# Kernel optimization log

Hardware: AMD Instinct MI355X
Metric: run time of the kernel (lower is better)

## Reference

```python
import jax, jax.numpy as jnp
import numpy as np

T, B, E, H = 2048, 2, 1024, 16
D = E // H

def setup_inputs() -> dict:
    key = jax.random.key(0)
    ks = jax.random.split(key, 5)
    s = 1.0 / np.sqrt(E)  # keep projection weights at sane scale
    return {
        "query": jax.random.normal(ks[0], (T, B, E), jnp.float32),
        "Wq": jax.random.normal(ks[1], (E, E), jnp.float32) * s,
        "bq": jnp.zeros((E,), jnp.float32),
        "Wk": jax.random.normal(ks[2], (E, E), jnp.float32) * s,
        "bk": jnp.zeros((E,), jnp.float32),
        "Wv": jax.random.normal(ks[3], (E, E), jnp.float32) * s,
        "bv": jnp.zeros((E,), jnp.float32),
        "Wo": jax.random.normal(ks[4], (E, E), jnp.float32) * s,
        "bo": jnp.zeros((E,), jnp.float32),
    }

def reference(query, Wq, bq, Wk, bk, Wv, bv, Wo, bo):
    # query: [T, B, E] (fairseq time-first). self-attention path.
    scaling = D ** -0.5
    q = (query @ Wq.T + bq) * scaling          # [T,B,E]
    k = query @ Wk.T + bk                      # [T,B,E]
    v = query @ Wv.T + bv                      # [T,B,E]
    # split heads: [T,B,H,D]
    q = q.reshape(T, B, H, D)
    k = k.reshape(T, B, H, D)
    v = v.reshape(T, B, H, D)
    # attention scores [B,H,T,S]
    scores = jnp.einsum("tbhd,sbhd->bhts", q, k)
    probs = jax.nn.softmax(scores, axis=-1)
    # weighted values -> [T,B,H,D]
    attn = jnp.einsum("bhts,sbhd->tbhd", probs, v).reshape(T, B, E)
    return attn @ Wo.T + bo                    # [T,B,E]
```

## Files before the change

kernel.cpp:

```cpp
#include <hip/hip_runtime.h>
#include <hip/hip_bf16.h>

#define T_DIM 2048

typedef __attribute__((ext_vector_type(8))) short short8_t;
typedef short8_t __attribute__((may_alias)) short8_a;
typedef __attribute__((ext_vector_type(4))) short short4_t;
typedef short4_t __attribute__((may_alias)) short4_a;
typedef __attribute__((ext_vector_type(4))) float f32x4;
typedef __attribute__((ext_vector_type(16))) float f32x16;
typedef __attribute__((ext_vector_type(4))) float float4_t;
typedef float4_t __attribute__((may_alias)) float4_a;
typedef __attribute__((ext_vector_type(4))) unsigned int u32x4;

__device__ __forceinline__ short f2bf(float f) {
    unsigned int u = __builtin_bit_cast(unsigned int, f);
    unsigned int r = (u + 0x7fffu + ((u >> 16) & 1u)) >> 16;
    return (short)r;
}

__device__ __forceinline__ void gl_lds16(const short* g, short* l) {
    __builtin_amdgcn_global_load_lds(
        (const __attribute__((address_space(1))) void*)g,
        (__attribute__((address_space(3))) void*)l, 16, 0, 0);
}

__global__ __launch_bounds__(256) void cvt_all(const float* __restrict__ query,
                                               const float* __restrict__ Wq,
                                               const float* __restrict__ Wk,
                                               const float* __restrict__ Wv,
                                               const float* __restrict__ Wo,
                                               short* __restrict__ out) {
    const int bx = blockIdx.x;
    const int i = bx * 2048 + threadIdx.x * 8;
    const float* s;
    if (bx < 2048) {
        s = query + i;
    } else {
        int j = i - 4194304;
        int wsel = j >> 20;
        const float* wp = wsel == 0 ? Wq : (wsel == 1 ? Wk : (wsel == 2 ? Wv : Wo));
        s = wp + (j & 1048575);
    }
    float4_a a = *(const float4_a*)s;
    float4_a b = *(const float4_a*)(s + 4);
    short8_a r;
    r[0] = f2bf(a[0]); r[1] = f2bf(a[1]); r[2] = f2bf(a[2]); r[3] = f2bf(a[3]);
    r[4] = f2bf(b[0]); r[5] = f2bf(b[1]); r[6] = f2bf(b[2]); r[7] = f2bf(b[3]);
    *(short8_a*)(out + i) = r;
}

template <int BM, int BN, int MODE>
__global__ __launch_bounds__(256) void gemm_lds(const short* __restrict__ A,
                                                const short* __restrict__ W,
                                                const float* __restrict__ b0,
                                                const float* __restrict__ b1,
                                                const float* __restrict__ b2,
                                                short* __restrict__ o0,
                                                short* __restrict__ o1,
                                                short* __restrict__ o2,
                                                float* __restrict__ of) {
    constexpr int FM = BM / 32;
    constexpr int FN = BN / 32;
    __shared__ short As[BM * 32];
    __shared__ short Bs[BN * 32];

    const int tid = threadIdx.x;
    const int l = tid & 63, w = tid >> 6;
    const int wm = w >> 1, wn = w & 1;

    const int nbx = gridDim.x;
    const int nb = nbx * gridDim.y;
    const int bid = blockIdx.x + nbx * blockIdx.y;
    const int swz = (bid & 7) * (nb >> 3) + (bid >> 3);
    const int bx = swz % nbx, by = swz / nbx;

    const int m0 = by * BM, n0 = bx * BN;
    const int l15 = l & 15, l4 = l >> 4;
    const int lr = l >> 2, lc = (l & 3) * 8;

    f32x4 acc[FM][FN];
#pragma unroll
    for (int i = 0; i < FM; i++)
#pragma unroll
        for (int j = 0; j < FN; j++) {
            f32x4 z = {0.f, 0.f, 0.f, 0.f};
            acc[i][j] = z;
        }

    const short* Ab = A + (m0 + lr) * 1024 + lc;
    const short* Wb = W + (n0 + lr) * 1024 + lc;

    for (int k0 = 0; k0 < 1024; k0 += 32) {
#pragma unroll
        for (int j = 0; j < BM / 64; j++) {
            int base = (j * 4 + w) * 16;
            gl_lds16(Ab + base * 1024 + k0, &As[base * 32]);
        }
#pragma unroll
        for (int j = 0; j < BN / 64; j++) {
            int base = (j * 4 + w) * 16;
            gl_lds16(Wb + base * 1024 + k0, &Bs[base * 32]);
        }
        __syncthreads();

        short8_t af[FM], bf[FN];
#pragma unroll
        for (int m = 0; m < FM; m++)
            af[m] = *(const short8_a*)&As[(wm * (BM / 2) + m * 16 + l15) * 32 + l4 * 8];
#pragma unroll
        for (int n = 0; n < FN; n++)
            bf[n] = *(const short8_a*)&Bs[(wn * (BN / 2) + n * 16 + l15) * 32 + l4 * 8];
#pragma unroll
        for (int m = 0; m < FM; m++)
#pragma unroll
            for (int n = 0; n < FN; n++)
                acc[m][n] = __builtin_amdgcn_mfma_f32_16x16x32_bf16(af[m], bf[n], acc[m][n], 0, 0, 0);
        __syncthreads();
    }

    if (MODE == 3) {
#pragma unroll
        for (int n = 0; n < FN; n++) {
            int col = n0 + wn * (BN / 2) + n * 16 + l15;
            float bv = b0[col];
#pragma unroll
            for (int m = 0; m < FM; m++)
#pragma unroll
                for (int i = 0; i < 4; i++) {
                    int row = m0 + wm * (BM / 2) + m * 16 + l4 * 4 + i;
                    of[row * 1024 + col] = acc[m][n][i] + bv;
                }
        }
    } else {
        const int proj = n0 >> 10;
        const float* bias = proj == 0 ? b0 : (proj == 1 ? b1 : b2);
        short* outp = proj == 0 ? o0 : (proj == 1 ? o1 : o2);
#pragma unroll
        for (int n = 0; n < FN; n++) {
            int cw = (n0 + wn * (BN / 2) + n * 16 + l15) & 1023;
            float bv = bias[cw];
            int h = cw >> 6, d = cw & 63;
#pragma unroll
            for (int m = 0; m < FM; m++)
#pragma unroll
                for (int i = 0; i < 4; i++) {
                    int row = m0 + wm * (BM / 2) + m * 16 + l4 * 4 + i;
                    float v = acc[m][n][i] + bv;
                    if (proj == 0) v *= 0.18033688011112042f;
                    int bb = row & 1, t = row >> 1;
                    if (proj == 2)
                        outp[((bb * 16 + h) * 64 + d) * 2048 + t] = f2bf(v);
                    else
                        outp[((bb * 16 + h) * 2048 + t) * 64 + d] = f2bf(v);
                }
        }
    }
}

__global__ __launch_bounds__(512, 4) void flash_attn(const short* __restrict__ Q,
                                                     const short* __restrict__ K,
                                                     const short* __restrict__ Vt,
                                                     short* __restrict__ O) {
    __shared__ short Ks[4][64 * 64];
    __shared__ short Vs[4][64 * 64];

    const int tid = threadIdx.x, l = tid & 63, w = tid >> 6;
    const int w4 = w >> 1, g = w & 1;
    const int l31 = l & 31, hi = l >> 5;
    const int e = l31 & 7;

    const int bid = blockIdx.x + (blockIdx.y << 4);
    const int swz = (bid & 7) * 64 + (bid >> 3);
    const int qt = swz & 15, bh = swz >> 4;

    const int b = bh >> 4, hh = bh & 15;
    const int qrow = qt * 128 + w4 * 32 + l31;

    const short* Qp = Q + bh * (T_DIM * 64);
    const short* Kp = K + bh * (T_DIM * 64);
    const short* Vp = Vt + bh * (64 * T_DIM);

    short8_t qf[4];
#pragma unroll
    for (int c = 0; c < 4; c++)
        qf[c] = *(const short8_a*)&Qp[qrow * 64 + c * 16 + hi * 8];

    f32x16 oacc[2];
    f32x16 lacc;
#pragma unroll
    for (int i = 0; i < 16; i++) { oacc[0][i] = 0.f; oacc[1][i] = 0.f; lacc[i] = 0.f; }

    short8_t ones;
#pragma unroll
    for (int j = 0; j < 8; j++) ones[j] = (short)0x3F80;

    const int lrow = l >> 3;
    const int lch = (l & 7) ^ (lrow & 7);
    const int wq = w & 3;
    const int j0 = 2 * wq, j1 = 2 * wq + 1;
    const short* sg0;
    const short* sg1;
    if (w < 4) {
        sg0 = Kp + (j0 * 8 + lrow) * 64 + lch * 8;
        sg1 = Kp + (j1 * 8 + lrow) * 64 + lch * 8;
    } else {
        sg0 = Vp + (j0 * 8 + lrow) * 2048 + lch * 8;
        sg1 = Vp + (j1 * 8 + lrow) * 2048 + lch * 8;
    }

    auto stage = [&](int t) {
        const int buf = t & 3;
        if (w < 4) {
            const int koff = t * 4096;
            gl_lds16(sg0 + koff, &Ks[buf][j0 * 512]);
            gl_lds16(sg1 + koff, &Ks[buf][j1 * 512]);
        } else {
            const int voff = t * 64;
            gl_lds16(sg0 + voff, &Vs[buf][j0 * 512]);
            gl_lds16(sg1 + voff, &Vs[buf][j1 * 512]);
        }
    };

    auto qk = [&](f32x16* st, int t) {
        const short* kc = &Ks[t & 3][0];
        f32x16 z;
#pragma unroll
        for (int i = 0; i < 16; i++) z[i] = 0.f;
        st[0] = z; st[1] = z;
#pragma unroll
        for (int c = 0; c < 4; c++) {
            short8_t kf0 = *(const short8_a*)&kc[(l31) * 64 + ((2 * c + hi) ^ e) * 8];
            short8_t kf1 = *(const short8_a*)&kc[(32 + l31) * 64 + ((2 * c + hi) ^ e) * 8];
            st[0] = __builtin_amdgcn_mfma_f32_32x32x16_bf16(kf0, qf[c], st[0], 0, 0, 0);
            st[1] = __builtin_amdgcn_mfma_f32_32x32x16_bf16(kf1, qf[c], st[1], 0, 0, 0);
        }
    };

    auto pv = [&](const short8_t* pf, int t) {
        const short* vc = &Vs[t & 3][0];
#pragma unroll
        for (int r = 0; r < 2; r++)
#pragma unroll
            for (int cc = 0; cc < 2; cc++) {
                short8_t p = pf[r * 2 + cc];
                lacc = __builtin_amdgcn_mfma_f32_32x32x16_bf16(ones, p, lacc, 0, 0, 0);
#pragma unroll
                for (int dd = 0; dd < 2; dd++) {
                    short8_t vf = *(const short8_a*)&vc[(dd * 32 + l31) * 64 +
                                                        ((4 * r + 2 * cc + hi) ^ e) * 8];
                    oacc[dd] = __builtin_amdgcn_mfma_f32_32x32x16_bf16(vf, p, oacc[dd], 0, 0, 0);
                }
            }
    };

    auto expack = [&](f32x16* st, short8_t* pf) {
#pragma unroll
        for (int r = 0; r < 2; r++) {
#pragma unroll
            for (int i = 0; i < 16; i++) st[r][i] = exp2f(st[r][i]);
            unsigned pk8[8];
#pragma unroll
            for (int u = 0; u < 8; u++) {
                unsigned t;
                asm("v_cvt_pk_bf16_f32 %0, %1, %2" : "=v"(t) : "v"(st[r][2 * u]), "v"(st[r][2 * u + 1]));
                pk8[u] = t;
            }
#pragma unroll
            for (int cc = 0; cc < 2; cc++) {
                unsigned A0 = pk8[4 * cc + 0], B0 = pk8[4 * cc + 2];
                unsigned A1 = pk8[4 * cc + 1], B1 = pk8[4 * cc + 3];
                asm("v_permlane32_swap_b32 %0, %1" : "+v"(A0), "+v"(B0));
                asm("v_permlane32_swap_b32 %0, %1" : "+v"(A1), "+v"(B1));
                u32x4 pu = {A0, A1, B0, B1};
                pf[r * 2 + cc] = __builtin_bit_cast(short8_t, pu);
            }
        }
    };

    stage(0);
    stage(1);

    f32x16 st[2];
    short8_t pf[4];

    for (int p = 0; p < 16; ++p) {
        __syncthreads();
        if (p < 15) { stage(2 * p + 2); stage(2 * p + 3); }
        const int t = 2 * p + g;
        __builtin_amdgcn_s_setprio(1);
        qk(st, t);
        __builtin_amdgcn_s_setprio(0);
        expack(st, pf);
        __builtin_amdgcn_s_setprio(1);
        pv(pf, t);
        __builtin_amdgcn_s_setprio(0);
    }

    __syncthreads();
    float* xo = (float*)&Ks[0][0];
    float* xml = (float*)&Vs[0][0];
    if (g == 1) {
#pragma unroll
        for (int dd = 0; dd < 2; dd++)
#pragma unroll
            for (int g4 = 0; g4 < 4; g4++) {
                f32x4 v = {oacc[dd][4 * g4], oacc[dd][4 * g4 + 1],
                           oacc[dd][4 * g4 + 2], oacc[dd][4 * g4 + 3]};
                *(float4_a*)&xo[w4 * 2048 + (dd * 4 + g4) * 256 + l * 4] = v;
            }
        xml[w4 * 64 + l] = lacc[0];
    }
    __syncthreads();
    if (g == 0) {
        float rl = 1.0f / (lacc[0] + xml[w4 * 64 + l]);
#pragma unroll
        for (int dd = 0; dd < 2; dd++)
#pragma unroll
            for (int g4 = 0; g4 < 4; g4++) {
                f32x4 o1 = *(const float4_a*)&xo[w4 * 2048 + (dd * 4 + g4) * 256 + l * 4];
                short4_t o4;
#pragma unroll
                for (int i = 0; i < 4; i++)
                    o4[i] = f2bf((oacc[dd][4 * g4 + i] + o1[i]) * rl);
                *(short4_a*)&O[(qrow * 2 + b) * 1024 + hh * 64 + dd * 32 + g4 * 8 + hi * 4] = o4;
            }
    }
}

extern "C" void kernel_launch(void* const* d_in, const int* in_sizes, int n_in,
                              void* d_out, int out_size, void* d_ws, size_t ws_size,
                              hipStream_t stream) {
    const float* query = (const float*)d_in[0];
    const float* Wq = (const float*)d_in[1];
    const float* bq = (const float*)d_in[2];
    const float* Wk = (const float*)d_in[3];
    const float* bk = (const float*)d_in[4];
    const float* Wv = (const float*)d_in[5];
    const float* bv = (const float*)d_in[6];
    const float* Wo = (const float*)d_in[7];
    const float* bo = (const float*)d_in[8];

    short* Xbf = (short*)d_ws;
    short* Wqb = Xbf + 4194304;
    short* Wkb = Wqb + 1048576;
    short* Wvb = Wkb + 1048576;
    short* Wob = Wvb + 1048576;
    short* Qb = Wob + 1048576;
    short* Kb = Qb + 4194304;
    short* Vtb = Kb + 4194304;
    short* attnb = Xbf;

    cvt_all<<<4096, 256, 0, stream>>>(query, Wq, Wk, Wv, Wo, Xbf);

    gemm_lds<128, 128, 4><<<dim3(24, 32), 256, 0, stream>>>(Xbf, Wqb, bq, bk, bv,
                                                            Qb, Kb, Vtb, nullptr);

    flash_attn<<<dim3(16, 32), 512, 0, stream>>>(Qb, Kb, Vtb, attnb);

    gemm_lds<64, 128, 3><<<dim3(8, 64), 256, 0, stream>>>(attnb, Wob, bo, nullptr, nullptr,
                                                          nullptr, nullptr, nullptr, (float*)d_out);
}
```

Measured before the change: 123.6 us.

## Pre-tile K/V into LDS-ready blocked layout and split QK into halves

The projection epilogue now writes K and V in a 64-row-tile, 8-element-chunked layout that matches the LDS fragment order. This lets flash attention stage tiles with contiguous global-to-LDS copies and read fragments without an XOR swizzle. The QK^T and exp/pack step is split into two 32-row halves that reuse one accumulator, which lowers register pressure. The risks are strided scattered global writes in the projection epilogue, possible LDS bank conflicts now that the swizzle is gone, and less MFMA overlap between the two halves.

```diff
diff --git a/kernel.cpp b/kernel.cpp
--- a/kernel.cpp
+++ b/kernel.cpp
@@ -149,10 +149,13 @@
                     float v = acc[m][n][i] + bv;
                     if (proj == 0) v *= 0.18033688011112042f;
                     int bb = row & 1, t = row >> 1;
-                    if (proj == 2)
-                        outp[((bb * 16 + h) * 64 + d) * 2048 + t] = f2bf(v);
+                    int bh = bb * 16 + h;
+                    if (proj == 0)
+                        outp[(bh * 2048 + t) * 64 + d] = f2bf(v);
+                    else if (proj == 1)
+                        outp[bh * 131072 + (t >> 6) * 4096 + (d >> 3) * 512 + (t & 63) * 8 + (d & 7)] = f2bf(v);
                     else
-                        outp[((bb * 16 + h) * 2048 + t) * 64 + d] = f2bf(v);
+                        outp[bh * 131072 + (t >> 6) * 4096 + ((t & 63) >> 3) * 512 + d * 8 + (t & 7)] = f2bf(v);
                 }
         }
     }
@@ -168,7 +171,6 @@
     const int tid = threadIdx.x, l = tid & 63, w = tid >> 6;
     const int w4 = w >> 1, g = w & 1;
     const int l31 = l & 31, hi = l >> 5;
-    const int e = l31 & 7;
 
     const int bid = blockIdx.x + (blockIdx.y << 4);
     const int swz = (bid & 7) * 64 + (bid >> 3);
@@ -178,8 +180,8 @@
     const int qrow = qt * 128 + w4 * 32 + l31;
 
     const short* Qp = Q + bh * (T_DIM * 64);
-    const short* Kp = K + bh * (T_DIM * 64);
-    const short* Vp = Vt + bh * (64 * T_DIM);
+    const short* Kp = K + bh * 131072;
+    const short* Vp = Vt + bh * 131072;
 
     short8_t qf[4];
 #pragma unroll
@@ -195,45 +197,58 @@
 #pragma unroll
     for (int j = 0; j < 8; j++) ones[j] = (short)0x3F80;
 
-    const int lrow = l >> 3;
-    const int lch = (l & 7) ^ (lrow & 7);
     const int wq = w & 3;
-    const int j0 = 2 * wq, j1 = 2 * wq + 1;
-    const short* sg0;
-    const short* sg1;
-    if (w < 4) {
-        sg0 = Kp + (j0 * 8 + lrow) * 64 + lch * 8;
-        sg1 = Kp + (j1 * 8 + lrow) * 64 + lch * 8;
-    } else {
-        sg0 = Vp + (j0 * 8 + lrow) * 2048 + lch * 8;
-        sg1 = Vp + (j1 * 8 + lrow) * 2048 + lch * 8;
-    }
+    const int p0 = 2 * wq, p1 = 2 * wq + 1;
+    const short* sgK0 = Kp + p0 * 512 + l * 8;
+    const short* sgK1 = Kp + p1 * 512 + l * 8;
+    const short* sgV0 = Vp + p0 * 512 + l * 8;
+    const short* sgV1 = Vp + p1 * 512 + l * 8;
 
     auto stage = [&](int t) {
-        const int buf = t & 3;
+        const int buf = t & 3, off = t * 4096;
         if (w < 4) {
-            const int koff = t * 4096;
-            gl_lds16(sg0 + koff, &Ks[buf][j0 * 512]);
-            gl_lds16(sg1 + koff, &Ks[buf][j1 * 512]);
+            gl_lds16(sgK0 + off, &Ks[buf][p0 * 512]);
+            gl_lds16(sgK1 + off, &Ks[buf][p1 * 512]);
         } else {
-            const int voff = t * 64;
-            gl_lds16(sg0 + voff, &Vs[buf][j0 * 512]);
-            gl_lds16(sg1 + voff, &Vs[buf][j1 * 512]);
+            gl_lds16(sgV0 + off, &Vs[buf][p0 * 512]);
+            gl_lds16(sgV1 + off, &Vs[buf][p1 * 512]);
         }
     };
 
-    auto qk = [&](f32x16* st, int t) {
+    auto qkhalf = [&](f32x16& s, int t, int r) {
         const short* kc = &Ks[t & 3][0];
-        f32x16 z;
-#pragma unroll
-        for (int i = 0; i < 16; i++) z[i] = 0.f;
-        st[0] = z; st[1] = z;
 #pragma unroll
         for (int c = 0; c < 4; c++) {
-            short8_t kf0 = *(const short8_a*)&kc[(l31) * 64 + ((2 * c + hi) ^ e) * 8];
-            short8_t kf1 = *(const short8_a*)&kc[(32 + l31) * 64 + ((2 * c + hi) ^ e) * 8];
-            st[0] = __builtin_amdgcn_mfma_f32_32x32x16_bf16(kf0, qf[c], st[0], 0, 0, 0);
-            st[1] = __builtin_amdgcn_mfma_f32_32x32x16_bf16(kf1, qf[c], st[1], 0, 0, 0);
+            short8_t kf = *(const short8_a*)&kc[(2 * c + hi) * 512 + (r * 32 + l31) * 8];
+            if (c == 0) {
+                f32x16 z;
+#pragma unroll
+                for (int i = 0; i < 16; i++) z[i] = 0.f;
+                s = __builtin_amdgcn_mfma_f32_32x32x16_bf16(kf, qf[0], z, 0, 0, 0);
+            } else {
+                s = __builtin_amdgcn_mfma_f32_32x32x16_bf16(kf, qf[c], s, 0, 0, 0);
+            }
+        }
+    };
+
+    auto expackhalf = [&](f32x16& s, short8_t* pf2) {
+#pragma unroll
+        for (int i = 0; i < 16; i++) s[i] = exp2f(s[i]);
+        unsigned pk8[8];
+#pragma unroll
+        for (int u = 0; u < 8; u++) {
+            unsigned t;
+            asm("v_cvt_pk_bf16_f32 %0, %1, %2" : "=v"(t) : "v"(s[2 * u]), "v"(s[2 * u + 1]));
+            pk8[u] = t;
+        }
+#pragma unroll
+        for (int cc = 0; cc < 2; cc++) {
+            unsigned A0 = pk8[4 * cc + 0], B0 = pk8[4 * cc + 2];
+            unsigned A1 = pk8[4 * cc + 1], B1 = pk8[4 * cc + 3];
+            asm("v_permlane32_swap_b32 %0, %1" : "+v"(A0), "+v"(B0));
+            asm("v_permlane32_swap_b32 %0, %1" : "+v"(A1), "+v"(B1));
+            u32x4 pu = {A0, A1, B0, B1};
+            pf2[cc] = __builtin_bit_cast(short8_t, pu);
         }
     };
 
@@ -247,41 +262,17 @@
                 lacc = __builtin_amdgcn_mfma_f32_32x32x16_bf16(ones, p, lacc, 0, 0, 0);
 #pragma unroll
                 for (int dd = 0; dd < 2; dd++) {
-                    short8_t vf = *(const short8_a*)&vc[(dd * 32 + l31) * 64 +
-                                                        ((4 * r + 2 * cc + hi) ^ e) * 8];
+                    short8_t vf = *(const short8_a*)&vc[(4 * r + 2 * cc + hi) * 512 +
+                                                        (dd * 32 + l31) * 8];
                     oacc[dd] = __builtin_amdgcn_mfma_f32_32x32x16_bf16(vf, p, oacc[dd], 0, 0, 0);
                 }
             }
     };
 
-    auto expack = [&](f32x16* st, short8_t* pf) {
-#pragma unroll
-        for (int r = 0; r < 2; r++) {
-#pragma unroll
-            for (int i = 0; i < 16; i++) st[r][i] = exp2f(st[r][i]);
-            unsigned pk8[8];
-#pragma unroll
-            for (int u = 0; u < 8; u++) {
-                unsigned t;
-                asm("v_cvt_pk_bf16_f32 %0, %1, %2" : "=v"(t) : "v"(st[r][2 * u]), "v"(st[r][2 * u + 1]));
-                pk8[u] = t;
-            }
-#pragma unroll
-            for (int cc = 0; cc < 2; cc++) {
-                unsigned A0 = pk8[4 * cc + 0], B0 = pk8[4 * cc + 2];
-                unsigned A1 = pk8[4 * cc + 1], B1 = pk8[4 * cc + 3];
-                asm("v_permlane32_swap_b32 %0, %1" : "+v"(A0), "+v"(B0));
-                asm("v_permlane32_swap_b32 %0, %1" : "+v"(A1), "+v"(B1));
-                u32x4 pu = {A0, A1, B0, B1};
-                pf[r * 2 + cc] = __builtin_bit_cast(short8_t, pu);
-            }
-        }
-    };
-
     stage(0);
     stage(1);
 
-    f32x16 st[2];
+    f32x16 s;
     short8_t pf[4];
 
     for (int p = 0; p < 16; ++p) {
@@ -289,9 +280,13 @@
         if (p < 15) { stage(2 * p + 2); stage(2 * p + 3); }
         const int t = 2 * p + g;
         __builtin_amdgcn_s_setprio(1);
-        qk(st, t);
+        qkhalf(s, t, 0);
         __builtin_amdgcn_s_setprio(0);
-        expack(st, pf);
+        expackhalf(s, &pf[0]);
+        __builtin_amdgcn_s_setprio(1);
+        qkhalf(s, t, 1);
+        __builtin_amdgcn_s_setprio(0);
+        expackhalf(s, &pf[2]);
         __builtin_amdgcn_s_setprio(1);
         pv(pf, t);
         __builtin_amdgcn_s_setprio(0);
```

Result: faster. 119.8 us (-3.1%).
